# Kernel optimization log

Hardware: AMD Instinct MI355X
Metric: run time of the kernel (lower is better)

## Reference

```python
import jax, jax.numpy as jnp
import numpy as np

FEATURE_NUM = 2048
TEMPERATURE = 0.5
EPS = 1e-12


def setup_inputs() -> dict:
    key = jax.random.key(0)
    k1, k2 = jax.random.split(key)
    B, N = 8192, FEATURE_NUM
    f1 = jax.random.uniform(k1, (B, N), dtype=jnp.float32)
    f2 = jax.random.uniform(k2, (B, N), dtype=jnp.float32)
    return {"f1": f1, "f2": f2}


def reference(f1, f2):
    N = FEATURE_NUM
    K = 2 * N
    # rows = features, cols = batch samples
    f = jnp.concatenate([f1.T, f2.T], axis=0)  # [K, B]

    # normalized entropy loss (predictions are sigmoid outputs in (0,1))
    ent = -f * jnp.log(f + EPS) - (1.0 - f) * jnp.log(1.0 - f + EPS)
    neloss = jnp.mean(ent) / jnp.log(2.0)

    # L2 normalize rows (torch F.normalize: x / max(||x||, eps))
    norm = jnp.linalg.norm(f, axis=1, keepdims=True)
    fn = f / jnp.maximum(norm, EPS)

    sim = (fn @ fn.T) / TEMPERATURE  # [K, K]

    # positives: off-diagonals at +/- N
    pos = jnp.concatenate([jnp.diagonal(sim, N), jnp.diagonal(sim, -N)])  # [K]

    # logits per row = [pos, negatives]; negatives = row minus main diag and +/-N diag.
    # logsumexp(pos U negatives) == logsumexp over the row excluding only the main diagonal,
    # since pos IS the +/-N diagonal entry of that row.
    diag_mask = jnp.eye(K, dtype=bool)
    lse = jax.nn.logsumexp(jnp.where(diag_mask, -jnp.inf, sim), axis=1)  # [K]

    # cross-entropy with label 0 (the positive slot), mean reduction
    ce = jnp.mean(lse - pos)
    return ce - neloss
```

## Files before the change

kernel.cpp:

```cpp
#include <hip/hip_runtime.h>
#include <math.h>

typedef __attribute__((ext_vector_type(4))) float f32x4;
typedef __attribute__((ext_vector_type(8))) short short8;
typedef unsigned int u32;

#define B_DIM 8192
#define N_FEAT 2048
#define K_ROWS 4096
#define INV_T 2.0f
#define EPSF 1e-12f

#define GT 96
#define GGRID 43
#define NTILES 946

#define FT_OFF    0ull
#define NORM2_OFF 67108864ull
#define INV_OFF   (NORM2_OFF + 16384)
#define RSUM_OFF  (INV_OFF + 32768)
#define PDOT_OFF  (RSUM_OFF + 16384)
#define ENT_OFF   (PDOT_OFF + 8192)
#define WS_END    (ENT_OFF + 2048)

__device__ __forceinline__ unsigned short f2bf(float x) {
  u32 u = __float_as_uint(x);
  u32 r = (u + 0x7fffu + ((u >> 16) & 1u)) >> 16;
  return (unsigned short)r;
}

__device__ __forceinline__ void gload16(const void* g, void* l) {
  __builtin_amdgcn_global_load_lds((const __attribute__((address_space(1))) u32*)g,
                                   (__attribute__((address_space(3))) u32*)l, 16, 0, 0);
}

__global__ __launch_bounds__(256) void stats_kernel(
    const float* __restrict__ f1, const float* __restrict__ f2,
    float* __restrict__ norm2, float* __restrict__ posdot,
    double* __restrict__ entpart) {
  const int col = blockIdx.x * 256 + threadIdx.x;
  const size_t base = (size_t)blockIdx.y * 64 * N_FEAT + col;
  const float* p1 = f1 + base;
  const float* p2 = f2 + base;
  float n1 = 0.f, n2 = 0.f, pd = 0.f, e0 = 0.f, e1 = 0.f;
#pragma unroll 8
  for (int r = 0; r < 64; ++r) {
    const float x = p1[(size_t)r * N_FEAT];
    const float y = p2[(size_t)r * N_FEAT];
    n1 += x * x; n2 += y * y; pd += x * y;
    e0 -= x * __log2f(x + EPSF) + (1.f - x) * __log2f(1.f - x + EPSF);
    e1 -= y * __log2f(y + EPSF) + (1.f - y) * __log2f(1.f - y + EPSF);
  }
  atomicAdd(&norm2[col], n1);
  atomicAdd(&norm2[N_FEAT + col], n2);
  atomicAdd(&posdot[col], pd);
  float ent = e0 + e1;
#pragma unroll
  for (int off = 1; off < 64; off <<= 1) ent += __shfl_xor(ent, off);
  if ((threadIdx.x & 63) == 0)
    atomicAdd(&entpart[(blockIdx.y * 8 + blockIdx.x + (threadIdx.x >> 6) * 64) & 255],
              (double)ent);
}

__global__ __launch_bounds__(256) void transpose_kernel(
    const float* __restrict__ f1, const float* __restrict__ f2,
    unsigned short* __restrict__ fT) {
  __shared__ float T1[64][65];
  __shared__ float T2[64][65];
  const int b0 = blockIdx.x * 64, k0 = blockIdx.y * 64;
  const int t = threadIdx.x;
  const int kq = t & 15, br = t >> 4;
#pragma unroll
  for (int rr = 0; rr < 4; ++rr) {
    const int b = br + rr * 16;
    const f32x4 v1 = *(const f32x4*)&f1[(size_t)(b0 + b) * N_FEAT + k0 + kq * 4];
    const f32x4 v2 = *(const f32x4*)&f2[(size_t)(b0 + b) * N_FEAT + k0 + kq * 4];
#pragma unroll
    for (int c = 0; c < 4; ++c) { T1[b][kq * 4 + c] = v1[c]; T2[b][kq * 4 + c] = v2[c]; }
  }
  __syncthreads();
  const int kl0 = t >> 3;
  const int b8 = (t & 7) * 8;
#pragma unroll
  for (int rr = 0; rr < 2; ++rr) {
    const int kl = rr * 32 + kl0;
    short8 o;
#pragma unroll
    for (int j = 0; j < 8; ++j) o[j] = (short)f2bf(T1[b8 + j][kl]);
    *(short8*)&fT[(size_t)(k0 + kl) * B_DIM + b0 + b8] = o;
#pragma unroll
    for (int j = 0; j < 8; ++j) o[j] = (short)f2bf(T2[b8 + j][kl]);
    *(short8*)&fT[(size_t)(N_FEAT + k0 + kl) * B_DIM + b0 + b8] = o;
  }
}

__global__ void inv_kernel(const float* __restrict__ norm2, float* __restrict__ inv) {
  const int i = blockIdx.x * 256 + threadIdx.x;
  if (i < K_ROWS) inv[i] = 1.f / fmaxf(sqrtf(norm2[i]), EPSF);
}

__global__ __launch_bounds__(256, 4) void gram_kernel(
    const unsigned short* __restrict__ fT, const float* __restrict__ inv,
    float* __restrict__ rowsum) {
  __shared__ __align__(16) unsigned short Al[GT * 64];
  __shared__ __align__(16) unsigned short Bl[GT * 64];
  const int orig = blockIdx.x;
  const int xcd = orig & 7;
  const int bid = (xcd < 2 ? xcd * 119 : 238 + (xcd - 2) * 118) + (orig >> 3);
  int r = (int)((sqrtf(8.f * (float)bid + 1.f) - 1.f) * 0.5f);
  while ((r + 1) * (r + 2) / 2 <= bid) ++r;
  while (r * (r + 1) / 2 > bid) --r;
  const int tj = r, ti = bid - r * (r + 1) / 2;

  const int t = threadIdx.x, lane = t & 63, wave = t >> 6;
  const int wr = wave >> 1, wc = wave & 1;
  const int Rb = wr * 48, Cb = wc * 48;
  const int rowl = lane & 15, lhi = lane >> 4;
  const int srow8 = wave * 8 + (lane >> 3);
  const int scol = (((lane & 7) ^ (lane >> 3)) * 8);
  const int tb = ti * GT, tjb = tj * GT;
  const bool diagT = (ti == tj);

  const unsigned short* pa[3];
  const unsigned short* pb[3];
#pragma unroll
  for (int it = 0; it < 3; ++it) {
    int ra = tb + it * 32 + srow8;  ra = ra < K_ROWS - 1 ? ra : K_ROWS - 1;
    int rb2 = tjb + it * 32 + srow8; rb2 = rb2 < K_ROWS - 1 ? rb2 : K_ROWS - 1;
    pa[it] = fT + (size_t)ra * B_DIM + scol;
    pb[it] = fT + (size_t)rb2 * B_DIM + scol;
  }

  f32x4 acc[3][3];
  const f32x4 zero = {0.f, 0.f, 0.f, 0.f};
#pragma unroll
  for (int m = 0; m < 3; ++m)
#pragma unroll
    for (int n = 0; n < 3; ++n) acc[m][n] = zero;

  for (int kt = 0; kt < B_DIM / 64; ++kt) {
    const size_t ko = (size_t)kt * 64;
#pragma unroll
    for (int it = 0; it < 3; ++it) {
      gload16(pa[it] + ko, &Al[(it * 32 + wave * 8) * 64]);
      gload16(pb[it] + ko, &Bl[(it * 32 + wave * 8) * 64]);
    }
    asm volatile("s_waitcnt vmcnt(0)" ::: "memory");
    __syncthreads();
#pragma unroll
    for (int kk = 0; kk < 64; kk += 32) {
      short8 af[3], bfv[3];
      const int sg = (kk >> 3) + lhi;
      const int so = ((sg ^ (rowl & 7)) << 3);
#pragma unroll
      for (int m = 0; m < 3; ++m)
        af[m] = *(const short8*)&Al[(Rb + m * 16 + rowl) * 64 + so];
#pragma unroll
      for (int n = 0; n < 3; ++n)
        bfv[n] = *(const short8*)&Bl[(Cb + n * 16 + rowl) * 64 + so];
#pragma unroll
      for (int m = 0; m < 3; ++m)
#pragma unroll
        for (int n = 0; n < 3; ++n)
          acc[m][n] = __builtin_amdgcn_mfma_f32_16x16x32_bf16(af[m], bfv[n], acc[m][n], 0, 0, 0);
    }
    __syncthreads();
  }

  float invj[3];
  bool cval[3];
#pragma unroll
  for (int n = 0; n < 3; ++n) {
    const int cg = tjb + Cb + n * 16 + rowl;
    cval[n] = cg < K_ROWS;
    invj[n] = inv[cg < K_ROWS ? cg : K_ROWS - 1];
  }
#pragma unroll
  for (int m = 0; m < 3; ++m) {
#pragma unroll
    for (int rg = 0; rg < 4; ++rg) {
      const int rloc = Rb + m * 16 + lhi * 4 + rg;
      const int rgl = tb + rloc;
      const bool rv = rgl < K_ROWS;
      const float invi = inv[rv ? rgl : K_ROWS - 1];
#pragma unroll
      for (int n = 0; n < 3; ++n) {
        const int cloc = Cb + n * 16 + rowl;
        const float e = __expf(acc[m][n][rg] * invi * invj[n] * INV_T);
        const bool keep = rv && cval[n] && !(diagT && rloc == cloc);
        acc[m][n][rg] = keep ? e : 0.f;
      }
    }
  }
#pragma unroll
  for (int m = 0; m < 3; ++m) {
#pragma unroll
    for (int rg = 0; rg < 4; ++rg) {
      float s = acc[m][0][rg] + acc[m][1][rg] + acc[m][2][rg];
      s += __shfl_xor(s, 1); s += __shfl_xor(s, 2);
      s += __shfl_xor(s, 4); s += __shfl_xor(s, 8);
      if (rowl == 0) {
        const int rgl = tb + Rb + m * 16 + lhi * 4 + rg;
        if (rgl < K_ROWS) atomicAdd(&rowsum[rgl], s);
      }
    }
  }
  if (!diagT) {
#pragma unroll
    for (int n = 0; n < 3; ++n) {
      float s = 0.f;
#pragma unroll
      for (int m = 0; m < 3; ++m)
#pragma unroll
        for (int rg = 0; rg < 4; ++rg) s += acc[m][n][rg];
      s += __shfl_xor(s, 16); s += __shfl_xor(s, 32);
      if (lhi == 0) {
        const int cg = tjb + Cb + n * 16 + rowl;
        if (cg < K_ROWS) atomicAdd(&rowsum[cg], s);
      }
    }
  }
}

__global__ __launch_bounds__(256) void final_kernel(
    const float* __restrict__ rowsum,
    const float* __restrict__ inv, const float* __restrict__ posdot,
    const double* __restrict__ entpart, float* __restrict__ out) {
  __shared__ double red[4];
  __shared__ double rede[4];
  const int t = threadIdx.x, lane = t & 63, wave = t >> 6;
  double ssum = 0.0;
  for (int i = t; i < K_ROWS; i += 256) {
    const float invi = inv[i];
    const float lse = __logf(rowsum[i]);
    const int ip = (i < N_FEAT) ? i : i - N_FEAT;
    const int io = (i < N_FEAT) ? i + N_FEAT : i - N_FEAT;
    const float pos = posdot[ip] * invi * inv[io] * INV_T;
    ssum += (double)(lse - pos);
  }
  double esum = entpart[t];
#pragma unroll
  for (int off = 1; off < 64; off <<= 1) {
    ssum += __shfl_xor(ssum, off);
    esum += __shfl_xor(esum, off);
  }
  if (lane == 0) { red[wave] = ssum; rede[wave] = esum; }
  __syncthreads();
  if (t == 0) {
    const double ce = (red[0] + red[1] + red[2] + red[3]) / (double)K_ROWS;
    const double etot = rede[0] + rede[1] + rede[2] + rede[3];
    const double nel = etot / ((double)K_ROWS * (double)B_DIM);
    out[0] = (float)(ce - nel);
  }
}

extern "C" void kernel_launch(void* const* d_in, const int* in_sizes, int n_in,
                              void* d_out, int out_size, void* d_ws, size_t ws_size,
                              hipStream_t stream) {
  const float* f1 = (const float*)d_in[0];
  const float* f2 = (const float*)d_in[1];
  char* ws = (char*)d_ws;
  unsigned short* fT = (unsigned short*)(ws + FT_OFF);
  float* norm2 = (float*)(ws + NORM2_OFF);
  float* inv = (float*)(ws + INV_OFF);
  float* rowsum = (float*)(ws + RSUM_OFF);
  float* posdot = (float*)(ws + PDOT_OFF);
  double* entpart = (double*)(ws + ENT_OFF);

  hipMemsetAsync(ws + NORM2_OFF, 0, (size_t)(WS_END - NORM2_OFF), stream);

  stats_kernel<<<dim3(N_FEAT / 256, 128), 256, 0, stream>>>(f1, f2, norm2, posdot, entpart);
  inv_kernel<<<K_ROWS / 256, 256, 0, stream>>>(norm2, inv);
  transpose_kernel<<<dim3(B_DIM / 64, N_FEAT / 64), 256, 0, stream>>>(f1, f2, fT);
  gram_kernel<<<NTILES, 256, 0, stream>>>(fT, inv, rowsum);
  final_kernel<<<1, 256, 0, stream>>>(rowsum, inv, posdot, entpart, (float*)d_out);
}
```

Before: 329.4 us.

## Fuse stats, inverse-norm and transpose kernels into a single prep pass

Folds the per-feature norm, positive-dot and entropy accumulation into the transpose kernel, so f1/f2 (128 MB of fp32) are read once instead of twice. The separate inv kernel is removed and inverse norms are recomputed from norm2 inside the gram and final kernels. This saves a full input read and two launches. In exchange the prep kernel issues many more atomics (one per feature per 64-row block, 128 blocks deep) and does extra log2 work inside the transpose path.

```diff
diff --git a/kernel.cpp b/kernel.cpp
--- a/kernel.cpp
+++ b/kernel.cpp
@@ -17,8 +17,7 @@
 
 #define FT_OFF    0ull
 #define NORM2_OFF 67108864ull
-#define INV_OFF   (NORM2_OFF + 16384)
-#define RSUM_OFF  (INV_OFF + 32768)
+#define RSUM_OFF  (NORM2_OFF + 16384)
 #define PDOT_OFF  (RSUM_OFF + 16384)
 #define ENT_OFF   (PDOT_OFF + 8192)
 #define WS_END    (ENT_OFF + 2048)
@@ -34,37 +33,10 @@
                                    (__attribute__((address_space(3))) u32*)l, 16, 0, 0);
 }
 
-__global__ __launch_bounds__(256) void stats_kernel(
+__global__ __launch_bounds__(256) void prep_kernel(
     const float* __restrict__ f1, const float* __restrict__ f2,
-    float* __restrict__ norm2, float* __restrict__ posdot,
-    double* __restrict__ entpart) {
-  const int col = blockIdx.x * 256 + threadIdx.x;
-  const size_t base = (size_t)blockIdx.y * 64 * N_FEAT + col;
-  const float* p1 = f1 + base;
-  const float* p2 = f2 + base;
-  float n1 = 0.f, n2 = 0.f, pd = 0.f, e0 = 0.f, e1 = 0.f;
-#pragma unroll 8
-  for (int r = 0; r < 64; ++r) {
-    const float x = p1[(size_t)r * N_FEAT];
-    const float y = p2[(size_t)r * N_FEAT];
-    n1 += x * x; n2 += y * y; pd += x * y;
-    e0 -= x * __log2f(x + EPSF) + (1.f - x) * __log2f(1.f - x + EPSF);
-    e1 -= y * __log2f(y + EPSF) + (1.f - y) * __log2f(1.f - y + EPSF);
-  }
-  atomicAdd(&norm2[col], n1);
-  atomicAdd(&norm2[N_FEAT + col], n2);
-  atomicAdd(&posdot[col], pd);
-  float ent = e0 + e1;
-#pragma unroll
-  for (int off = 1; off < 64; off <<= 1) ent += __shfl_xor(ent, off);
-  if ((threadIdx.x & 63) == 0)
-    atomicAdd(&entpart[(blockIdx.y * 8 + blockIdx.x + (threadIdx.x >> 6) * 64) & 255],
-              (double)ent);
-}
-
-__global__ __launch_bounds__(256) void transpose_kernel(
-    const float* __restrict__ f1, const float* __restrict__ f2,
-    unsigned short* __restrict__ fT) {
+    unsigned short* __restrict__ fT, float* __restrict__ norm2,
+    float* __restrict__ posdot, double* __restrict__ entpart) {
   __shared__ float T1[64][65];
   __shared__ float T2[64][65];
   const int b0 = blockIdx.x * 64, k0 = blockIdx.y * 64;
@@ -81,26 +53,42 @@
   __syncthreads();
   const int kl0 = t >> 3;
   const int b8 = (t & 7) * 8;
+  float ent = 0.f;
 #pragma unroll
   for (int rr = 0; rr < 2; ++rr) {
     const int kl = rr * 32 + kl0;
-    short8 o;
-#pragma unroll
-    for (int j = 0; j < 8; ++j) o[j] = (short)f2bf(T1[b8 + j][kl]);
-    *(short8*)&fT[(size_t)(k0 + kl) * B_DIM + b0 + b8] = o;
-#pragma unroll
-    for (int j = 0; j < 8; ++j) o[j] = (short)f2bf(T2[b8 + j][kl]);
-    *(short8*)&fT[(size_t)(N_FEAT + k0 + kl) * B_DIM + b0 + b8] = o;
-  }
-}
-
-__global__ void inv_kernel(const float* __restrict__ norm2, float* __restrict__ inv) {
-  const int i = blockIdx.x * 256 + threadIdx.x;
-  if (i < K_ROWS) inv[i] = 1.f / fmaxf(sqrtf(norm2[i]), EPSF);
+    float n1 = 0.f, n2 = 0.f, pd = 0.f;
+    short8 o1v, o2v;
+#pragma unroll
+    for (int j = 0; j < 8; ++j) {
+      const float x = T1[b8 + j][kl];
+      const float y = T2[b8 + j][kl];
+      n1 += x * x; n2 += y * y; pd += x * y;
+      ent -= x * __log2f(x + EPSF) + (1.f - x) * __log2f(1.f - x + EPSF);
+      ent -= y * __log2f(y + EPSF) + (1.f - y) * __log2f(1.f - y + EPSF);
+      o1v[j] = (short)f2bf(x);
+      o2v[j] = (short)f2bf(y);
+    }
+    *(short8*)&fT[(size_t)(k0 + kl) * B_DIM + b0 + b8] = o1v;
+    *(short8*)&fT[(size_t)(N_FEAT + k0 + kl) * B_DIM + b0 + b8] = o2v;
+    n1 += __shfl_xor(n1, 1); n1 += __shfl_xor(n1, 2); n1 += __shfl_xor(n1, 4);
+    n2 += __shfl_xor(n2, 1); n2 += __shfl_xor(n2, 2); n2 += __shfl_xor(n2, 4);
+    pd += __shfl_xor(pd, 1); pd += __shfl_xor(pd, 2); pd += __shfl_xor(pd, 4);
+    if ((t & 7) == 0) {
+      atomicAdd(&norm2[k0 + kl], n1);
+      atomicAdd(&norm2[N_FEAT + k0 + kl], n2);
+      atomicAdd(&posdot[k0 + kl], pd);
+    }
+  }
+#pragma unroll
+  for (int off = 1; off < 64; off <<= 1) ent += __shfl_xor(ent, off);
+  if ((t & 63) == 0)
+    atomicAdd(&entpart[(blockIdx.x * 37 + blockIdx.y * 5 + (t >> 6)) & 255],
+              (double)ent);
 }
 
 __global__ __launch_bounds__(256, 4) void gram_kernel(
-    const unsigned short* __restrict__ fT, const float* __restrict__ inv,
+    const unsigned short* __restrict__ fT, const float* __restrict__ norm2,
     float* __restrict__ rowsum) {
   __shared__ __align__(16) unsigned short Al[GT * 64];
   __shared__ __align__(16) unsigned short Bl[GT * 64];
@@ -173,7 +161,7 @@
   for (int n = 0; n < 3; ++n) {
     const int cg = tjb + Cb + n * 16 + rowl;
     cval[n] = cg < K_ROWS;
-    invj[n] = inv[cg < K_ROWS ? cg : K_ROWS - 1];
+    invj[n] = 1.f / fmaxf(sqrtf(norm2[cg < K_ROWS ? cg : K_ROWS - 1]), EPSF);
   }
 #pragma unroll
   for (int m = 0; m < 3; ++m) {
@@ -182,7 +170,7 @@
       const int rloc = Rb + m * 16 + lhi * 4 + rg;
       const int rgl = tb + rloc;
       const bool rv = rgl < K_ROWS;
-      const float invi = inv[rv ? rgl : K_ROWS - 1];
+      const float invi = 1.f / fmaxf(sqrtf(norm2[rv ? rgl : K_ROWS - 1]), EPSF);
 #pragma unroll
       for (int n = 0; n < 3; ++n) {
         const int cloc = Cb + n * 16 + rowl;
@@ -223,19 +211,20 @@
 }
 
 __global__ __launch_bounds__(256) void final_kernel(
-    const float* __restrict__ rowsum,
-    const float* __restrict__ inv, const float* __restrict__ posdot,
-    const double* __restrict__ entpart, float* __restrict__ out) {
+    const float* __restrict__ rowsum, const float* __restrict__ norm2,
+    const float* __restrict__ posdot, const double* __restrict__ entpart,
+    float* __restrict__ out) {
   __shared__ double red[4];
   __shared__ double rede[4];
   const int t = threadIdx.x, lane = t & 63, wave = t >> 6;
   double ssum = 0.0;
   for (int i = t; i < K_ROWS; i += 256) {
-    const float invi = inv[i];
+    const float invi = 1.f / fmaxf(sqrtf(norm2[i]), EPSF);
     const float lse = __logf(rowsum[i]);
     const int ip = (i < N_FEAT) ? i : i - N_FEAT;
     const int io = (i < N_FEAT) ? i + N_FEAT : i - N_FEAT;
-    const float pos = posdot[ip] * invi * inv[io] * INV_T;
+    const float invo = 1.f / fmaxf(sqrtf(norm2[io]), EPSF);
+    const float pos = posdot[ip] * invi * invo * INV_T;
     ssum += (double)(lse - pos);
   }
   double esum = entpart[t];
@@ -262,16 +251,13 @@
   char* ws = (char*)d_ws;
   unsigned short* fT = (unsigned short*)(ws + FT_OFF);
   float* norm2 = (float*)(ws + NORM2_OFF);
-  float* inv = (float*)(ws + INV_OFF);
   float* rowsum = (float*)(ws + RSUM_OFF);
   float* posdot = (float*)(ws + PDOT_OFF);
   double* entpart = (double*)(ws + ENT_OFF);
 
   hipMemsetAsync(ws + NORM2_OFF, 0, (size_t)(WS_END - NORM2_OFF), stream);
 
-  stats_kernel<<<dim3(N_FEAT / 256, 128), 256, 0, stream>>>(f1, f2, norm2, posdot, entpart);
-  inv_kernel<<<K_ROWS / 256, 256, 0, stream>>>(norm2, inv);
-  transpose_kernel<<<dim3(B_DIM / 64, N_FEAT / 64), 256, 0, stream>>>(f1, f2, fT);
-  gram_kernel<<<NTILES, 256, 0, stream>>>(fT, inv, rowsum);
-  final_kernel<<<1, 256, 0, stream>>>(rowsum, inv, posdot, entpart, (float*)d_out);
-}
+  prep_kernel<<<dim3(B_DIM / 64, N_FEAT / 64), 256, 0, stream>>>(f1, f2, fT, norm2, posdot, entpart);
+  gram_kernel<<<NTILES, 256, 0, stream>>>(fT, norm2, rowsum);
+  final_kernel<<<1, 256, 0, stream>>>(rowsum, norm2, posdot, entpart, (float*)d_out);
+}
```

Result: no change. 325.3 us (-1.2%).
